# Optimization experiments

Hardware: AMD Instinct MI355X
Metric: run time of the kernel (lower is better)

The kernel has to match this reference:

```python
import jax, jax.numpy as jnp
import numpy as np
from jax import lax

B, T, D = 8, 4096, 512
UNITS = 512
WINDOW = 2


def setup_inputs() -> dict:
    key = jax.random.key(0)
    k1, k2, k3 = jax.random.split(key, 3)
    x = jax.random.normal(k1, (B, T, D), dtype=jnp.float32)
    # keras kernel shape is (window, 1, input_dim, 3*units); drop the dummy height dim
    kernel = jax.random.uniform(k2, (WINDOW, D, 3 * UNITS), dtype=jnp.float32,
                                minval=-0.05, maxval=0.05)
    bias = jnp.zeros((3 * UNITS,), dtype=jnp.float32)
    return {"x": x, "kernel": kernel, "bias": bias}


def reference(x, kernel, bias):
    window, d_in, u3 = kernel.shape
    units = u3 // 3
    # causal padding: window-1 zeros on the left of the time axis
    xp = jnp.pad(x, ((0, 0), (window - 1, 0), (0, 0)))
    # 1D valid conv -> gates [B, T, 3*units]
    gates = lax.conv_general_dilated(
        xp, kernel, window_strides=(1,), padding='VALID',
        dimension_numbers=('NWC', 'WIO', 'NWC')) + bias
    z = jnp.tanh(gates[..., :units])
    f = jax.nn.sigmoid(gates[..., units:2 * units])
    o = jax.nn.sigmoid(gates[..., 2 * units:])

    # fo-pool recurrence: c_t = f_t * c_{t-1} + (1 - f_t) * z_t ; out_t = o_t * c_t
    def step(c, zfo):
        z_t, f_t, o_t = zfo
        c = f_t * c + (1.0 - f_t) * z_t
        return c, o_t * c

    c0 = jnp.zeros((x.shape[0], units), dtype=x.dtype)
    zT = jnp.swapaxes(z, 0, 1)  # [T, B, U]
    fT = jnp.swapaxes(f, 0, 1)
    oT = jnp.swapaxes(o, 0, 1)
    _, ysT = lax.scan(step, c0, (zT, fT, oT))
    return jnp.swapaxes(ysT, 0, 1)  # [B, T, U] (return_sequences=True)
```

## Files before the change

kernel.cpp:

```cpp
#include <hip/hip_runtime.h>
#include <cstdint>
#include <cstddef>

#define BB   8
#define TT   4096
#define DD   512
#define UU   512
#define NN   1536
#define KK   1024
#define MM   32768
#define NCH  256
#define CHL  16

using bf16x8 = __attribute__((ext_vector_type(8))) __bf16;
using f32x4  = __attribute__((ext_vector_type(4))) float;

__device__ __forceinline__ unsigned short f2bf(float f) {
    unsigned u = __float_as_uint(f);
    u += 0x7fffu + ((u >> 16) & 1u);
    return (unsigned short)(u >> 16);
}
__device__ __forceinline__ float bf2f(unsigned short s) {
    return __uint_as_float(((unsigned)s) << 16);
}
__device__ __forceinline__ float sigf(float x) { return 1.0f / (1.0f + __expf(-x)); }
__device__ __forceinline__ float tanh_(float x) { return 1.0f - 2.0f / (1.0f + __expf(2.0f * x)); }

__device__ __forceinline__ void async16(const void* g, void* l) {
    __builtin_amdgcn_global_load_lds(
        (__attribute__((address_space(1))) void*)g,
        (__attribute__((address_space(3))) void*)l, 16, 0, 0);
}

__global__ void k_prep(const float* __restrict__ x, unsigned short* __restrict__ xpad,
                       const float* __restrict__ kern, unsigned short* __restrict__ kT) {
    int bx = blockIdx.x;
    int by = blockIdx.y;
    int tid = threadIdx.x;
    if (bx < 2049) {
        int q = bx * 256 + tid;
        if (q >= 4097 * 128) return;
        int tp = q >> 7;
        int d  = (q & 127) << 2;
        size_t oi = ((size_t)by * 4097 + tp) * 512 + d;
        ushort4 o;
        if (tp == 0) {
            o.x = o.y = o.z = o.w = 0;
        } else {
            float4 v = *(const float4*)(x + ((size_t)by * 4096 + (tp - 1)) * 512 + d);
            o.x = f2bf(v.x); o.y = f2bf(v.y); o.z = f2bf(v.z); o.w = f2bf(v.w);
        }
        *(ushort4*)(xpad + oi) = o;
    } else {
        __shared__ float tile[32][33];
        int idx = (bx - 2049) * 8 + by;
        int c  = tid & 31;
        int r0 = tid >> 5;
        for (int t8 = 0; t8 < 8; ++t8) {
            int tnum = idx * 8 + t8;
            int k0 = (tnum & 31) * 32;
            int n0 = (tnum >> 5) * 32;
#pragma unroll
            for (int rr = r0; rr < 32; rr += 8)
                tile[rr][c] = kern[(size_t)(k0 + rr) * NN + n0 + c];
            __syncthreads();
#pragma unroll
            for (int rr = r0; rr < 32; rr += 8)
                kT[(size_t)(n0 + rr) * KK + k0 + c] = f2bf(tile[c][rr]);
            __syncthreads();
        }
    }
}


#define STAGE_A(BUF, KT, KH) do { \
    async16(xpad + abase + (size_t)rowS0 * 512 + ((KT) * 64 + (KH) * 32 + kcS0), \
            smem + (BUF) * 65536 + (KH) * 16384 + offL0); \
    async16(xpad + abase + (size_t)rowS1 * 512 + ((KT) * 64 + (KH) * 32 + kcS1), \
            smem + (BUF) * 65536 + (KH) * 16384 + offL1); \
} while (0)

#define STAGE_B(BUF, KT, KH) do { \
    async16(kTg + (size_t)(n0 + rowS0) * 1024 + ((KT) * 64 + (KH) * 32 + kcS0), \
            smem + (BUF) * 65536 + 32768 + (KH) * 16384 + offL0); \
    async16(kTg + (size_t)(n0 + rowS1) * 1024 + ((KT) * 64 + (KH) * 32 + kcS1), \
            smem + (BUF) * 65536 + 32768 + (KH) * 16384 + offL1); \
} while (0)

#define VM4 asm volatile("s_waitcnt vmcnt(4)" ::: "memory")
#define VM0 asm volatile("s_waitcnt vmcnt(0)" ::: "memory")

#define LDS_A(BUF, KS, MR) (*(const bf16x8*)(smem + (BUF) * 65536 + (KS) * 16384 + (MR) * 1024 + ldsA))
#define LDS_B(BUF, KS, NR) (*(const bf16x8*)(smem + (BUF) * 65536 + (KS) * 16384 + (NR) * 1024 + ldsB))

#define PHASE(BUF, MH, KS, LB, STG, VMW) \
    af[0] = LDS_A(BUF, KS, (MH) * 4 + 0); \
    af[1] = LDS_A(BUF, KS, (MH) * 4 + 1); \
    af[2] = LDS_A(BUF, KS, (MH) * 4 + 2); \
    af[3] = LDS_A(BUF, KS, (MH) * 4 + 3); \
    if (LB) { \
        bf[0] = LDS_B(BUF, KS, 0); \
        bf[1] = LDS_B(BUF, KS, 1); \
        bf[2] = LDS_B(BUF, KS, 2); \
        bf[3] = LDS_B(BUF, KS, 3); \
    } \
    STG; \
    __builtin_amdgcn_s_barrier(); \
    __builtin_amdgcn_s_setprio(1); \
    acc[(MH)*4+0][0] = __builtin_amdgcn_mfma_f32_16x16x32_bf16(af[0], bf[0], acc[(MH)*4+0][0], 0, 0, 0); \
    acc[(MH)*4+0][1] = __builtin_amdgcn_mfma_f32_16x16x32_bf16(af[0], bf[1], acc[(MH)*4+0][1], 0, 0, 0); \
    acc[(MH)*4+0][2] = __builtin_amdgcn_mfma_f32_16x16x32_bf16(af[0], bf[2], acc[(MH)*4+0][2], 0, 0, 0); \
    acc[(MH)*4+0][3] = __builtin_amdgcn_mfma_f32_16x16x32_bf16(af[0], bf[3], acc[(MH)*4+0][3], 0, 0, 0); \
    acc[(MH)*4+1][0] = __builtin_amdgcn_mfma_f32_16x16x32_bf16(af[1], bf[0], acc[(MH)*4+1][0], 0, 0, 0); \
    acc[(MH)*4+1][1] = __builtin_amdgcn_mfma_f32_16x16x32_bf16(af[1], bf[1], acc[(MH)*4+1][1], 0, 0, 0); \
    acc[(MH)*4+1][2] = __builtin_amdgcn_mfma_f32_16x16x32_bf16(af[1], bf[2], acc[(MH)*4+1][2], 0, 0, 0); \
    acc[(MH)*4+1][3] = __builtin_amdgcn_mfma_f32_16x16x32_bf16(af[1], bf[3], acc[(MH)*4+1][3], 0, 0, 0); \
    acc[(MH)*4+2][0] = __builtin_amdgcn_mfma_f32_16x16x32_bf16(af[2], bf[0], acc[(MH)*4+2][0], 0, 0, 0); \
    acc[(MH)*4+2][1] = __builtin_amdgcn_mfma_f32_16x16x32_bf16(af[2], bf[1], acc[(MH)*4+2][1], 0, 0, 0); \
    acc[(MH)*4+2][2] = __builtin_amdgcn_mfma_f32_16x16x32_bf16(af[2], bf[2], acc[(MH)*4+2][2], 0, 0, 0); \
    acc[(MH)*4+2][3] = __builtin_amdgcn_mfma_f32_16x16x32_bf16(af[2], bf[3], acc[(MH)*4+2][3], 0, 0, 0); \
    acc[(MH)*4+3][0] = __builtin_amdgcn_mfma_f32_16x16x32_bf16(af[3], bf[0], acc[(MH)*4+3][0], 0, 0, 0); \
    acc[(MH)*4+3][1] = __builtin_amdgcn_mfma_f32_16x16x32_bf16(af[3], bf[1], acc[(MH)*4+3][1], 0, 0, 0); \
    acc[(MH)*4+3][2] = __builtin_amdgcn_mfma_f32_16x16x32_bf16(af[3], bf[2], acc[(MH)*4+3][2], 0, 0, 0); \
    acc[(MH)*4+3][3] = __builtin_amdgcn_mfma_f32_16x16x32_bf16(af[3], bf[3], acc[(MH)*4+3][3], 0, 0, 0); \
    __builtin_amdgcn_s_setprio(0); \
    VMW; \
    __builtin_amdgcn_s_barrier();

__global__ __launch_bounds__(512, 2) void k_gemm(
    const unsigned short* __restrict__ xpad,
    const unsigned short* __restrict__ kTg,
    const float* __restrict__ bias,
    unsigned short* __restrict__ gates)
{
    __shared__ char smem[131072];

    const int tid  = threadIdx.x;
    const int wid  = tid >> 6;
    const int lane = tid & 63;
    const int wr   = wid >> 2;
    const int wc   = wid & 3;
    const int lrow = lane & 15;
    const int quad = lane >> 4;

    const int bid = blockIdx.x;
    const int wg  = (bid & 7) * 96 + (bid >> 3);
    const int mt  = wg / 6;
    const int nt  = wg % 6;
    const int m0  = mt * 256;
    const int n0  = nt * 256;
    const int boff = m0 >> 12;
    const size_t abase = (size_t)(m0 + boff) * 512;

    const int off0 = (wid * 2 + 0) * 1024 + lane * 16;
    const int off1 = (wid * 2 + 1) * 1024 + lane * 16;
    const int ln0 = off0 >> 7, ln1 = off1 >> 7;
    const int g80 = ((off0 >> 4) & 7) ^ (ln0 & 7);
    const int g81 = ((off1 >> 4) & 7) ^ (ln1 & 7);
    const int offL0 = off0, offL1 = off1;
    const int rowS0 = ln0 * 2 + (g80 >> 2), rowS1 = ln1 * 2 + (g81 >> 2);
    const int kcS0 = (g80 & 3) * 8,         kcS1 = (g81 & 3) * 8;

    const int lh  = lrow >> 1;
    const int g8f = ((lrow & 1) * 4 + quad) ^ lh;
    const int ldsA = (wr * 64 + lh) * 128 + g8f * 16;
    const int ldsB = 32768 + (wc * 32 + lh) * 128 + g8f * 16;

    f32x4 acc[8][4] = {};
    bf16x8 af[4], bf[4];

    STAGE_A(0, 0, 0); STAGE_B(0, 0, 0); STAGE_A(0, 0, 1); STAGE_B(0, 0, 1);
    VM4;
    __builtin_amdgcn_s_barrier();

    for (int i = 0; i < 7; ++i) {
        const int t1 = 2 * i + 1;
        const int t2 = 2 * i + 2;
        PHASE(0, 0, 0, 1, STAGE_A(1, t1, 0), (void)0)
        PHASE(0, 1, 0, 0, STAGE_B(1, t1, 0), VM4)
        PHASE(0, 0, 1, 1, STAGE_A(1, t1, 1), (void)0)
        PHASE(0, 1, 1, 0, STAGE_B(1, t1, 1), VM4)
        PHASE(1, 0, 0, 1, STAGE_A(0, t2, 0), (void)0)
        PHASE(1, 1, 0, 0, STAGE_B(0, t2, 0), VM4)
        PHASE(1, 0, 1, 1, STAGE_A(0, t2, 1), (void)0)
        PHASE(1, 1, 1, 0, STAGE_B(0, t2, 1), VM4)
    }
    {
        PHASE(0, 0, 0, 1, STAGE_A(1, 15, 0), (void)0)
        PHASE(0, 1, 0, 0, STAGE_B(1, 15, 0), VM4)
        PHASE(0, 0, 1, 1, STAGE_A(1, 15, 1), (void)0)
        PHASE(0, 1, 1, 0, STAGE_B(1, 15, 1), VM4)
        PHASE(1, 0, 0, 1, (void)0, (void)0)
        PHASE(1, 1, 0, 0, (void)0, VM0)
        PHASE(1, 0, 1, 1, (void)0, (void)0)
        PHASE(1, 1, 1, 0, (void)0, (void)0)
    }

#pragma unroll
    for (int n = 0; n < 4; ++n) {
        int coll = wc * 64 + n * 16 + lrow;
        float bv = bias[n0 + coll];
        int g    = coll >> 3;
        int cb   = (coll & 7) * 2;
#pragma unroll
        for (int m = 0; m < 8; ++m) {
            int rbase = wr * 128 + m * 16 + quad * 4;
#pragma unroll
            for (int r = 0; r < 4; ++r) {
                int row = rbase + r;
                *(unsigned short*)(smem + row * 512 + ((g ^ (row & 7)) * 16) + cb)
                    = f2bf(acc[m][n][r] + bv);
            }
        }
    }
    __syncthreads();
    {
        unsigned short* gbase = gates + (size_t)m0 * NN + n0;
#pragma unroll
        for (int it = 0; it < 16; ++it) {
            int idx = it * 512 + tid;
            int row = idx >> 5;
            int g   = idx & 31;
            bf16x8 v = *(const bf16x8*)(smem + row * 512 + ((g ^ (row & 7)) * 16));
            *(bf16x8*)(gbase + (size_t)row * NN + g * 8) = v;
        }
    }
}

__global__ __launch_bounds__(128) void k_scanA(const unsigned short* __restrict__ gates,
                        float* __restrict__ Fp, float* __restrict__ Ce) {
    const int chunk = blockIdx.x;
    const int b     = blockIdx.y;
    const int u     = threadIdx.x << 2;
    const size_t g0 = ((size_t)b * TT + (size_t)chunk * CHL) * NN + u;

    float c0 = 0, c1 = 0, c2 = 0, c3 = 0;
    float F0 = 1, F1 = 1, F2 = 1, F3 = 1;

    ushort4 bz[8], bf_[8];
#pragma unroll
    for (int j = 0; j < 8; ++j) {
        bz[j]  = *(const ushort4*)(gates + g0 + (size_t)j * NN);
        bf_[j] = *(const ushort4*)(gates + g0 + (size_t)j * NN + UU);
    }
#pragma unroll
    for (int h = 0; h < 2; ++h) {
        ushort4 nz[8], nf[8];
        if (h == 0) {
#pragma unroll
            for (int j = 0; j < 8; ++j) {
                nz[j] = *(const ushort4*)(gates + g0 + (size_t)(8 + j) * NN);
                nf[j] = *(const ushort4*)(gates + g0 + (size_t)(8 + j) * NN + UU);
            }
        }
#pragma unroll
        for (int j = 0; j < 8; ++j) {
            float f0 = sigf(bf2f(bf_[j].x)), z0 = tanh_(bf2f(bz[j].x));
            float f1 = sigf(bf2f(bf_[j].y)), z1 = tanh_(bf2f(bz[j].y));
            float f2 = sigf(bf2f(bf_[j].z)), z2 = tanh_(bf2f(bz[j].z));
            float f3 = sigf(bf2f(bf_[j].w)), z3 = tanh_(bf2f(bz[j].w));
            c0 = f0 * c0 + (1.0f - f0) * z0; F0 *= f0;
            c1 = f1 * c1 + (1.0f - f1) * z1; F1 *= f1;
            c2 = f2 * c2 + (1.0f - f2) * z2; F2 *= f2;
            c3 = f3 * c3 + (1.0f - f3) * z3; F3 *= f3;
        }
        if (h == 0) {
#pragma unroll
            for (int j = 0; j < 8; ++j) { bz[j] = nz[j]; bf_[j] = nf[j]; }
        }
    }
    size_t ci = ((size_t)b * NCH + chunk) * UU + u;
    *(float4*)(Fp + ci) = make_float4(F0, F1, F2, F3);
    *(float4*)(Ce + ci) = make_float4(c0, c1, c2, c3);
}

__global__ __launch_bounds__(128) void k_scanB(const float* __restrict__ Fp,
                        const float* __restrict__ Ce, float* __restrict__ Cin) {
    int gid = blockIdx.x * 128 + threadIdx.x;
    int bb = gid >> 9;
    int uu = gid & 511;
    size_t base = (size_t)bb * NCH * UU + uu;
    float c = 0.0f;
    for (int k0 = 0; k0 < NCH; k0 += 8) {
        float F[8], E[8];
#pragma unroll
        for (int j = 0; j < 8; ++j) {
            F[j] = Fp[base + (size_t)(k0 + j) * UU];
            E[j] = Ce[base + (size_t)(k0 + j) * UU];
        }
#pragma unroll
        for (int j = 0; j < 8; ++j) {
            Cin[base + (size_t)(k0 + j) * UU] = c;
            c = F[j] * c + E[j];
        }
    }
}

__global__ __launch_bounds__(128) void k_scanC(const unsigned short* __restrict__ gates,
                        const float* __restrict__ Cin, float* __restrict__ out) {
    const int chunk = blockIdx.x;
    const int b     = blockIdx.y;
    const int u     = threadIdx.x << 2;
    const size_t g0 = ((size_t)b * TT + (size_t)chunk * CHL) * NN + u;
    size_t o = ((size_t)b * TT + (size_t)chunk * CHL) * UU + u;

    size_t ci = ((size_t)b * NCH + chunk) * UU + u;
    float4 cv = *(const float4*)(Cin + ci);
    float c0 = cv.x, c1 = cv.y, c2 = cv.z, c3 = cv.w;

    ushort4 bz[4], bf_[4], bo[4];
#pragma unroll
    for (int j = 0; j < 4; ++j) {
        bz[j]  = *(const ushort4*)(gates + g0 + (size_t)j * NN);
        bf_[j] = *(const ushort4*)(gates + g0 + (size_t)j * NN + UU);
        bo[j]  = *(const ushort4*)(gates + g0 + (size_t)j * NN + 2 * UU);
    }
#pragma unroll
    for (int k = 0; k < 4; ++k) {
        ushort4 nz[4], nf[4], no[4];
        if (k < 3) {
#pragma unroll
            for (int j = 0; j < 4; ++j) {
                size_t gg = g0 + (size_t)((k + 1) * 4 + j) * NN;
                nz[j] = *(const ushort4*)(gates + gg);
                nf[j] = *(const ushort4*)(gates + gg + UU);
                no[j] = *(const ushort4*)(gates + gg + 2 * UU);
            }
        }
#pragma unroll
        for (int j = 0; j < 4; ++j) {
            float f0 = sigf(bf2f(bf_[j].x)), z0 = tanh_(bf2f(bz[j].x)), o0 = sigf(bf2f(bo[j].x));
            float f1 = sigf(bf2f(bf_[j].y)), z1 = tanh_(bf2f(bz[j].y)), o1 = sigf(bf2f(bo[j].y));
            float f2 = sigf(bf2f(bf_[j].z)), z2 = tanh_(bf2f(bz[j].z)), o2 = sigf(bf2f(bo[j].z));
            float f3 = sigf(bf2f(bf_[j].w)), z3 = tanh_(bf2f(bz[j].w)), o3 = sigf(bf2f(bo[j].w));
            c0 = f0 * c0 + (1.0f - f0) * z0;
            c1 = f1 * c1 + (1.0f - f1) * z1;
            c2 = f2 * c2 + (1.0f - f2) * z2;
            c3 = f3 * c3 + (1.0f - f3) * z3;
            f32x4 ov = { o0 * c0, o1 * c1, o2 * c2, o3 * c3 };
            __builtin_nontemporal_store(ov, (f32x4*)(out + o));
            o += UU;
        }
        if (k < 3) {
#pragma unroll
            for (int j = 0; j < 4; ++j) { bz[j] = nz[j]; bf_[j] = nf[j]; bo[j] = no[j]; }
        }
    }
}

extern "C" void kernel_launch(void* const* d_in, const int* in_sizes, int n_in,
                              void* d_out, int out_size, void* d_ws, size_t ws_size,
                              hipStream_t stream) {
    const float* x    = (const float*)d_in[0];
    const float* kern = (const float*)d_in[1];
    const float* bias = (const float*)d_in[2];
    float* out = (float*)d_out;
    char* ws = (char*)d_ws;

    unsigned short* xpad  = (unsigned short*)(ws + 0);
    unsigned short* kT    = (unsigned short*)(ws + 33562624);
    unsigned short* gates = (unsigned short*)(ws + 36708352);
    float* Fp  = (float*)(ws + 137371648);
    float* Ce  = (float*)(ws + 141565952);
    float* Cin = (float*)(ws + 145760256);

    hipLaunchKernelGGL(k_prep,  dim3(2049 + 24, 8), dim3(256), 0, stream, x, xpad, kern, kT);
    hipLaunchKernelGGL(k_gemm,  dim3(768),          dim3(512), 0, stream, xpad, kT, bias, gates);
    hipLaunchKernelGGL(k_scanA, dim3(NCH, BB),      dim3(128), 0, stream, gates, Fp, Ce);
    hipLaunchKernelGGL(k_scanB, dim3(32),           dim3(128), 0, stream, Fp, Ce, Cin);
    hipLaunchKernelGGL(k_scanC, dim3(NCH, BB),      dim3(128), 0, stream, gates, Cin, out);
}
```

Before: 310.0 us.

## Double-buffer MFMA operand registers to prefetch next LDS fragments during compute

Restructures the GEMM main loop so each phase reads the next phase's A/B fragments from LDS into a second register set while issuing MFMAs on the current set. The two barriers per phase become one, with a sched_barrier to keep LDS reads ahead of the MFMAs, and the vmcnt waits are retimed to VM2 on alternate phases. The aim is to hide LDS read latency and cut barrier overhead. In exchange it uses more VGPRs under the 512x2 launch bound and carries hazards around buffer reuse and wait ordering.

```diff
diff --git a/kernel.cpp b/kernel.cpp
--- a/kernel.cpp
+++ b/kernel.cpp
@@ -88,44 +88,47 @@
 } while (0)
 
 #define VM4 asm volatile("s_waitcnt vmcnt(4)" ::: "memory")
+#define VM2 asm volatile("s_waitcnt vmcnt(2)" ::: "memory")
 #define VM0 asm volatile("s_waitcnt vmcnt(0)" ::: "memory")
 
 #define LDS_A(BUF, KS, MR) (*(const bf16x8*)(smem + (BUF) * 65536 + (KS) * 16384 + (MR) * 1024 + ldsA))
 #define LDS_B(BUF, KS, NR) (*(const bf16x8*)(smem + (BUF) * 65536 + (KS) * 16384 + (NR) * 1024 + ldsB))
 
-#define PHASE(BUF, MH, KS, LB, STG, VMW) \
-    af[0] = LDS_A(BUF, KS, (MH) * 4 + 0); \
-    af[1] = LDS_A(BUF, KS, (MH) * 4 + 1); \
-    af[2] = LDS_A(BUF, KS, (MH) * 4 + 2); \
-    af[3] = LDS_A(BUF, KS, (MH) * 4 + 3); \
-    if (LB) { \
-        bf[0] = LDS_B(BUF, KS, 0); \
-        bf[1] = LDS_B(BUF, KS, 1); \
-        bf[2] = LDS_B(BUF, KS, 2); \
-        bf[3] = LDS_B(BUF, KS, 3); \
+#define PH(DO_R, RBUF, RKS, RMH, AFN, LBN, BFN, AFC, BFC, MH, STG, VMW) \
+    __builtin_amdgcn_s_barrier(); \
+    if (DO_R) { \
+        AFN[0] = LDS_A(RBUF, RKS, (RMH) * 4 + 0); \
+        AFN[1] = LDS_A(RBUF, RKS, (RMH) * 4 + 1); \
+        AFN[2] = LDS_A(RBUF, RKS, (RMH) * 4 + 2); \
+        AFN[3] = LDS_A(RBUF, RKS, (RMH) * 4 + 3); \
+        if (LBN) { \
+            BFN[0] = LDS_B(RBUF, RKS, 0); \
+            BFN[1] = LDS_B(RBUF, RKS, 1); \
+            BFN[2] = LDS_B(RBUF, RKS, 2); \
+            BFN[3] = LDS_B(RBUF, RKS, 3); \
+        } \
     } \
     STG; \
-    __builtin_amdgcn_s_barrier(); \
+    __builtin_amdgcn_sched_barrier(0); \
     __builtin_amdgcn_s_setprio(1); \
-    acc[(MH)*4+0][0] = __builtin_amdgcn_mfma_f32_16x16x32_bf16(af[0], bf[0], acc[(MH)*4+0][0], 0, 0, 0); \
-    acc[(MH)*4+0][1] = __builtin_amdgcn_mfma_f32_16x16x32_bf16(af[0], bf[1], acc[(MH)*4+0][1], 0, 0, 0); \
-    acc[(MH)*4+0][2] = __builtin_amdgcn_mfma_f32_16x16x32_bf16(af[0], bf[2], acc[(MH)*4+0][2], 0, 0, 0); \
-    acc[(MH)*4+0][3] = __builtin_amdgcn_mfma_f32_16x16x32_bf16(af[0], bf[3], acc[(MH)*4+0][3], 0, 0, 0); \
-    acc[(MH)*4+1][0] = __builtin_amdgcn_mfma_f32_16x16x32_bf16(af[1], bf[0], acc[(MH)*4+1][0], 0, 0, 0); \
-    acc[(MH)*4+1][1] = __builtin_amdgcn_mfma_f32_16x16x32_bf16(af[1], bf[1], acc[(MH)*4+1][1], 0, 0, 0); \
-    acc[(MH)*4+1][2] = __builtin_amdgcn_mfma_f32_16x16x32_bf16(af[1], bf[2], acc[(MH)*4+1][2], 0, 0, 0); \
-    acc[(MH)*4+1][3] = __builtin_amdgcn_mfma_f32_16x16x32_bf16(af[1], bf[3], acc[(MH)*4+1][3], 0, 0, 0); \
-    acc[(MH)*4+2][0] = __builtin_amdgcn_mfma_f32_16x16x32_bf16(af[2], bf[0], acc[(MH)*4+2][0], 0, 0, 0); \
-    acc[(MH)*4+2][1] = __builtin_amdgcn_mfma_f32_16x16x32_bf16(af[2], bf[1], acc[(MH)*4+2][1], 0, 0, 0); \
-    acc[(MH)*4+2][2] = __builtin_amdgcn_mfma_f32_16x16x32_bf16(af[2], bf[2], acc[(MH)*4+2][2], 0, 0, 0); \
-    acc[(MH)*4+2][3] = __builtin_amdgcn_mfma_f32_16x16x32_bf16(af[2], bf[3], acc[(MH)*4+2][3], 0, 0, 0); \
-    acc[(MH)*4+3][0] = __builtin_amdgcn_mfma_f32_16x16x32_bf16(af[3], bf[0], acc[(MH)*4+3][0], 0, 0, 0); \
-    acc[(MH)*4+3][1] = __builtin_amdgcn_mfma_f32_16x16x32_bf16(af[3], bf[1], acc[(MH)*4+3][1], 0, 0, 0); \
-    acc[(MH)*4+3][2] = __builtin_amdgcn_mfma_f32_16x16x32_bf16(af[3], bf[2], acc[(MH)*4+3][2], 0, 0, 0); \
-    acc[(MH)*4+3][3] = __builtin_amdgcn_mfma_f32_16x16x32_bf16(af[3], bf[3], acc[(MH)*4+3][3], 0, 0, 0); \
+    acc[(MH)*4+0][0] = __builtin_amdgcn_mfma_f32_16x16x32_bf16(AFC[0], BFC[0], acc[(MH)*4+0][0], 0, 0, 0); \
+    acc[(MH)*4+0][1] = __builtin_amdgcn_mfma_f32_16x16x32_bf16(AFC[0], BFC[1], acc[(MH)*4+0][1], 0, 0, 0); \
+    acc[(MH)*4+0][2] = __builtin_amdgcn_mfma_f32_16x16x32_bf16(AFC[0], BFC[2], acc[(MH)*4+0][2], 0, 0, 0); \
+    acc[(MH)*4+0][3] = __builtin_amdgcn_mfma_f32_16x16x32_bf16(AFC[0], BFC[3], acc[(MH)*4+0][3], 0, 0, 0); \
+    acc[(MH)*4+1][0] = __builtin_amdgcn_mfma_f32_16x16x32_bf16(AFC[1], BFC[0], acc[(MH)*4+1][0], 0, 0, 0); \
+    acc[(MH)*4+1][1] = __builtin_amdgcn_mfma_f32_16x16x32_bf16(AFC[1], BFC[1], acc[(MH)*4+1][1], 0, 0, 0); \
+    acc[(MH)*4+1][2] = __builtin_amdgcn_mfma_f32_16x16x32_bf16(AFC[1], BFC[2], acc[(MH)*4+1][2], 0, 0, 0); \
+    acc[(MH)*4+1][3] = __builtin_amdgcn_mfma_f32_16x16x32_bf16(AFC[1], BFC[3], acc[(MH)*4+1][3], 0, 0, 0); \
+    acc[(MH)*4+2][0] = __builtin_amdgcn_mfma_f32_16x16x32_bf16(AFC[2], BFC[0], acc[(MH)*4+2][0], 0, 0, 0); \
+    acc[(MH)*4+2][1] = __builtin_amdgcn_mfma_f32_16x16x32_bf16(AFC[2], BFC[1], acc[(MH)*4+2][1], 0, 0, 0); \
+    acc[(MH)*4+2][2] = __builtin_amdgcn_mfma_f32_16x16x32_bf16(AFC[2], BFC[2], acc[(MH)*4+2][2], 0, 0, 0); \
+    acc[(MH)*4+2][3] = __builtin_amdgcn_mfma_f32_16x16x32_bf16(AFC[2], BFC[3], acc[(MH)*4+2][3], 0, 0, 0); \
+    acc[(MH)*4+3][0] = __builtin_amdgcn_mfma_f32_16x16x32_bf16(AFC[3], BFC[0], acc[(MH)*4+3][0], 0, 0, 0); \
+    acc[(MH)*4+3][1] = __builtin_amdgcn_mfma_f32_16x16x32_bf16(AFC[3], BFC[1], acc[(MH)*4+3][1], 0, 0, 0); \
+    acc[(MH)*4+3][2] = __builtin_amdgcn_mfma_f32_16x16x32_bf16(AFC[3], BFC[2], acc[(MH)*4+3][2], 0, 0, 0); \
+    acc[(MH)*4+3][3] = __builtin_amdgcn_mfma_f32_16x16x32_bf16(AFC[3], BFC[3], acc[(MH)*4+3][3], 0, 0, 0); \
     __builtin_amdgcn_s_setprio(0); \
-    VMW; \
-    __builtin_amdgcn_s_barrier();
+    VMW;
 
 __global__ __launch_bounds__(512, 2) void k_gemm(
     const unsigned short* __restrict__ xpad,
@@ -167,35 +170,40 @@
     const int ldsB = 32768 + (wc * 32 + lh) * 128 + g8f * 16;
 
     f32x4 acc[8][4] = {};
-    bf16x8 af[4], bf[4];
+    bf16x8 afS0[4], afS1[4], bfS0[4], bfS1[4];
 
     STAGE_A(0, 0, 0); STAGE_B(0, 0, 0); STAGE_A(0, 0, 1); STAGE_B(0, 0, 1);
     VM4;
     __builtin_amdgcn_s_barrier();
+    afS0[0] = LDS_A(0, 0, 0); afS0[1] = LDS_A(0, 0, 1);
+    afS0[2] = LDS_A(0, 0, 2); afS0[3] = LDS_A(0, 0, 3);
+    bfS0[0] = LDS_B(0, 0, 0); bfS0[1] = LDS_B(0, 0, 1);
+    bfS0[2] = LDS_B(0, 0, 2); bfS0[3] = LDS_B(0, 0, 3);
 
     for (int i = 0; i < 7; ++i) {
         const int t1 = 2 * i + 1;
         const int t2 = 2 * i + 2;
-        PHASE(0, 0, 0, 1, STAGE_A(1, t1, 0), (void)0)
-        PHASE(0, 1, 0, 0, STAGE_B(1, t1, 0), VM4)
-        PHASE(0, 0, 1, 1, STAGE_A(1, t1, 1), (void)0)
-        PHASE(0, 1, 1, 0, STAGE_B(1, t1, 1), VM4)
-        PHASE(1, 0, 0, 1, STAGE_A(0, t2, 0), (void)0)
-        PHASE(1, 1, 0, 0, STAGE_B(0, t2, 0), VM4)
-        PHASE(1, 0, 1, 1, STAGE_A(0, t2, 1), (void)0)
-        PHASE(1, 1, 1, 0, STAGE_B(0, t2, 1), VM4)
+        PH(1, 0, 0, 1, afS1, 0, bfS0, afS0, bfS0, 0, STAGE_A(1, t1, 0), VM2)
+        PH(1, 0, 1, 0, afS0, 1, bfS1, afS1, bfS0, 1, STAGE_B(1, t1, 0), (void)0)
+        PH(1, 0, 1, 1, afS1, 0, bfS0, afS0, bfS1, 0, STAGE_A(1, t1, 1), VM2)
+        PH(1, 1, 0, 0, afS0, 1, bfS0, afS1, bfS1, 1, STAGE_B(1, t1, 1), (void)0)
+        PH(1, 1, 0, 1, afS1, 0, bfS0, afS0, bfS0, 0, STAGE_A(0, t2, 0), VM2)
+        PH(1, 1, 1, 0, afS0, 1, bfS1, afS1, bfS0, 1, STAGE_B(0, t2, 0), (void)0)
+        PH(1, 1, 1, 1, afS1, 0, bfS0, afS0, bfS1, 0, STAGE_A(0, t2, 1), VM2)
+        PH(1, 0, 0, 0, afS0, 1, bfS0, afS1, bfS1, 1, STAGE_B(0, t2, 1), (void)0)
     }
     {
-        PHASE(0, 0, 0, 1, STAGE_A(1, 15, 0), (void)0)
-        PHASE(0, 1, 0, 0, STAGE_B(1, 15, 0), VM4)
-        PHASE(0, 0, 1, 1, STAGE_A(1, 15, 1), (void)0)
-        PHASE(0, 1, 1, 0, STAGE_B(1, 15, 1), VM4)
-        PHASE(1, 0, 0, 1, (void)0, (void)0)
-        PHASE(1, 1, 0, 0, (void)0, VM0)
-        PHASE(1, 0, 1, 1, (void)0, (void)0)
-        PHASE(1, 1, 1, 0, (void)0, (void)0)
-    }
-
+        PH(1, 0, 0, 1, afS1, 0, bfS0, afS0, bfS0, 0, STAGE_A(1, 15, 0), VM2)
+        PH(1, 0, 1, 0, afS0, 1, bfS1, afS1, bfS0, 1, STAGE_B(1, 15, 0), (void)0)
+        PH(1, 0, 1, 1, afS1, 0, bfS0, afS0, bfS1, 0, STAGE_A(1, 15, 1), VM2)
+        PH(1, 1, 0, 0, afS0, 1, bfS0, afS1, bfS1, 1, STAGE_B(1, 15, 1), (void)0)
+        PH(1, 1, 0, 1, afS1, 0, bfS0, afS0, bfS0, 0, (void)0,           VM0)
+        PH(1, 1, 1, 0, afS0, 1, bfS1, afS1, bfS0, 1, (void)0,           (void)0)
+        PH(1, 1, 1, 1, afS1, 0, bfS0, afS0, bfS1, 0, (void)0,           (void)0)
+        PH(0, 0, 0, 0, afS0, 0, bfS0, afS1, bfS1, 1, (void)0,           (void)0)
+    }
+
+    __syncthreads();
 #pragma unroll
     for (int n = 0; n < 4; ++n) {
         int coll = wc * 64 + n * 16 + lrow;
```

After: 309.8 us, median of 2. About the same (-0.1%).
